# Performance work log

Measured on AMD Instinct MI355X. Metric: run time of the kernel, lower is better.

Reference implementation:

```python
import jax, jax.numpy as jnp
import numpy as np

N = 131072      # total nodes across batched graphs
E = 524288      # total directed edges (avg degree 4, molecular graphs)
F_NODE = 64     # raw atom features
F_BOND = 16     # raw bond features
D = 128         # hidden width (hard-coded in the module)
H2 = 16
G = 4096        # number of graphs in the batch
DIM_OUT = 1


def _make_params(key):
    ks = iter(jax.random.split(key, 64))
    def w(shape, scale):
        return jax.random.normal(next(ks), shape, jnp.float32) * scale
    p = {"fc1_w": w((F_NODE, D), 0.1), "fc1_b": jnp.zeros((D,), jnp.float32)}
    for l in (1, 2, 3):
        p[f"gc{l}_wq"] = w((D, D), 0.05); p[f"gc{l}_bq"] = jnp.zeros((D,), jnp.float32)
        p[f"gc{l}_wk"] = w((D, D), 0.05); p[f"gc{l}_bk"] = jnp.zeros((D,), jnp.float32)
        p[f"gc{l}_wv"] = w((D, D), 0.05); p[f"gc{l}_bv"] = jnp.zeros((D,), jnp.float32)
        p[f"gc{l}_we"] = w((F_BOND, D), 0.05)   # PyG lin_edge has no bias
        p[f"gc{l}_ws"] = w((D, D), 0.05); p[f"gc{l}_bs"] = jnp.zeros((D,), jnp.float32)
    p["fc2_w"] = w((D, H2), 0.1); p["fc2_b"] = jnp.zeros((H2,), jnp.float32)
    p["fc3_w"] = w((H2, DIM_OUT), 0.1); p["fc3_b"] = jnp.zeros((DIM_OUT,), jnp.float32)
    return p


def setup_inputs() -> dict:
    key = jax.random.key(0)
    k1, k2, k3, k4, kp = jax.random.split(key, 5)
    inp = {
        "x": jax.random.normal(k1, (N, F_NODE), jnp.float32),
        "edge_index": jax.random.randint(k2, (2, E), 0, N),
        "edge_attr": jax.random.normal(k3, (E, F_BOND), jnp.float32),
        "batch": jnp.sort(jax.random.randint(k4, (N,), 0, G)),
    }
    inp.update(_make_params(kp))
    return inp


def _tconv(x, src, dst, edge_attr, wq, bq, wk, bk, wv, bv, we, ws, bs):
    # PyG TransformerConv, heads=1, concat=True, beta=False, root_weight=True
    n = x.shape[0]
    q = x @ wq + bq                                   # [N,D]
    k = x @ wk + bk                                   # [N,D]
    v = x @ wv + bv                                   # [N,D]
    e = edge_attr @ we                                # [E,D] edge projection
    kj = k[src] + e                                   # key_j + edge
    vj = v[src] + e                                   # value_j + edge
    alpha = jnp.sum(q[dst] * kj, axis=-1) / jnp.sqrt(jnp.float32(D))   # [E]
    # segment softmax over incoming edges of each dst node
    amax = jax.ops.segment_max(alpha, dst, num_segments=n)
    ex = jnp.exp(alpha - amax[dst])
    denom = jax.ops.segment_sum(ex, dst, num_segments=n)
    w = ex / denom[dst]                               # [E]
    agg = jax.ops.segment_sum(vj * w[:, None], dst, num_segments=n)    # scatter-add
    return agg + x @ ws + bs                          # skip / root weight


def reference(x, edge_index, edge_attr, batch,
              fc1_w, fc1_b,
              gc1_wq, gc1_bq, gc1_wk, gc1_bk, gc1_wv, gc1_bv, gc1_we, gc1_ws, gc1_bs,
              gc2_wq, gc2_bq, gc2_wk, gc2_bk, gc2_wv, gc2_bv, gc2_we, gc2_ws, gc2_bs,
              gc3_wq, gc3_bq, gc3_wk, gc3_bk, gc3_wv, gc3_bv, gc3_we, gc3_ws, gc3_bs,
              fc2_w, fc2_b, fc3_w, fc3_b):
    src, dst = edge_index[0], edge_index[1]
    h = x @ fc1_w + fc1_b
    layers = [
        (gc1_wq, gc1_bq, gc1_wk, gc1_bk, gc1_wv, gc1_bv, gc1_we, gc1_ws, gc1_bs),
        (gc2_wq, gc2_bq, gc2_wk, gc2_bk, gc2_wv, gc2_bv, gc2_we, gc2_ws, gc2_bs),
        (gc3_wq, gc3_bq, gc3_wk, gc3_bk, gc3_wv, gc3_bv, gc3_we, gc3_ws, gc3_bs),
    ]
    for p in layers:
        h = jax.nn.relu(_tconv(h, src, dst, edge_attr, *p))
    # global mean pool over graph ids
    cnt = jax.ops.segment_sum(jnp.ones((h.shape[0],), h.dtype), batch, num_segments=G)
    hg = jax.ops.segment_sum(h, batch, num_segments=G) / jnp.maximum(cnt, 1.0)[:, None]
    h = jax.nn.relu(hg @ fc2_w + fc2_b)
    return h @ fc3_w + fc3_b                          # [G, DIM_OUT]
```

## Files before the change

### kernel.cpp

```cpp
#include <hip/hip_runtime.h>
#include <hip/hip_fp16.h>


#define D 128

typedef _Float16 half8 __attribute__((ext_vector_type(8)));
typedef float f32x4 __attribute__((ext_vector_type(4)));

__global__ __launch_bounds__(256) void hist_kernel(const int* __restrict__ dst,
                                                   int* __restrict__ counts, int e) {
  int i = blockIdx.x * 256 + threadIdx.x;
  if (i < e) atomicAdd(&counts[dst[i]], 1);
}

__global__ __launch_bounds__(256) void scan_a_kernel(const int* __restrict__ counts,
                                                     int* __restrict__ incl,
                                                     int* __restrict__ bsum) {
  int gid = blockIdx.x * 256 + threadIdx.x;
  int lane = threadIdx.x & 63, wid = threadIdx.x >> 6;
  int v = counts[gid];
  int s = v;
  #pragma unroll
  for (int off = 1; off < 64; off <<= 1) {
    int t = __shfl_up(s, off, 64);
    if (lane >= off) s += t;
  }
  __shared__ int wsum[4];
  if (lane == 63) wsum[wid] = s;
  __syncthreads();
  #pragma unroll
  for (int w = 0; w < 3; ++w)
    if (wid > w) s += wsum[w];
  incl[gid] = s;
  if (threadIdx.x == 255) bsum[blockIdx.x] = s;
}

__global__ __launch_bounds__(512) void scan_b_kernel(int* __restrict__ bs) {
  int tid = threadIdx.x;
  int lane = tid & 63, wid = tid >> 6;
  int v = bs[tid];
  int s = v;
  #pragma unroll
  for (int off = 1; off < 64; off <<= 1) {
    int t = __shfl_up(s, off, 64);
    if (lane >= off) s += t;
  }
  __shared__ int wsum[8];
  if (lane == 63) wsum[wid] = s;
  __syncthreads();
  #pragma unroll
  for (int w = 0; w < 7; ++w)
    if (wid > w) s += wsum[w];
  bs[tid] = s - v;
}

__global__ __launch_bounds__(256) void scan_c_kernel(const int* __restrict__ incl,
                                                     const int* __restrict__ counts,
                                                     const int* __restrict__ bsum,
                                                     int* __restrict__ offs, int n, int e) {
  int gid = blockIdx.x * 256 + threadIdx.x;
  if (gid < n) offs[gid] = incl[gid] - counts[gid] + bsum[blockIdx.x];
  if (gid == 0) offs[n] = e;
}

__global__ __launch_bounds__(256) void scatter_kernel(const int* __restrict__ srcs,
                                                      const int* __restrict__ dsts,
                                                      const int* __restrict__ offs,
                                                      int* __restrict__ cursor,
                                                      int* __restrict__ csr_src,
                                                      int* __restrict__ csr_eid, int e) {
  int i = blockIdx.x * 256 + threadIdx.x;
  if (i >= e) return;
  int d = dsts[i];
  int slot = atomicAdd(&cursor[d], 1);
  int p = offs[d] + slot;
  csr_src[p] = srcs[i];
  csr_eid[p] = i;
}

__global__ __launch_bounds__(256) void sort_kernel(const int* __restrict__ offs,
                                                   int* __restrict__ eid,
                                                   int* __restrict__ srcs, int n) {
  int i = blockIdx.x * 256 + threadIdx.x;
  if (i >= n) return;
  int b = offs[i], e = offs[i + 1];
  for (int p = b + 1; p < e; ++p) {
    int ke = eid[p], ks = srcs[p];
    int q = p - 1;
    while (q >= b && eid[q] > ke) {
      eid[q + 1] = eid[q]; srcs[q + 1] = srcs[q]; --q;
    }
    eid[q + 1] = ke; srcs[q + 1] = ks;
  }
}

__global__ __launch_bounds__(256) void convw_kernel(const float* __restrict__ W,
                                                    __half* __restrict__ out,
                                                    int ncols, int K) {
  int idx = blockIdx.x * 256 + threadIdx.x;
  if (idx >= ncols * K) return;
  int n = idx / K, kk = idx - n * K;
  out[idx] = __float2half(W[(size_t)kk * ncols + n]);
}

__global__ __launch_bounds__(256) void convwe_kernel(const float* __restrict__ we,
                                                     const float* __restrict__ Wq,
                                                     const float* __restrict__ bq,
                                                     __half* __restrict__ outW,
                                                     float* __restrict__ outB) {
  int idx = blockIdx.x * 256 + threadIdx.x;
  if (idx < 2048) {
    int f = idx >> 7, kk = idx & 127;
    float s = 0.f;
    for (int d = 0; d < 128; ++d) s += we[f * 128 + d] * Wq[kk * 128 + d];
    outW[f * 128 + kk] = __float2half(s);
  } else if (idx < 2064) {
    int f = idx - 2048;
    float s = 0.f;
    for (int d = 0; d < 128; ++d) s += we[f * 128 + d] * bq[d];
    outB[f] = s;
  }
}

__global__ __launch_bounds__(256) void bcat_kernel(const float* __restrict__ bq,
                                                   const float* __restrict__ bk,
                                                   const float* __restrict__ bv,
                                                   const float* __restrict__ bs,
                                                   float* __restrict__ out) {
  int j = blockIdx.x * 256 + threadIdx.x;
  if (j >= 512) return;
  const float* src = (j < 128) ? bq : (j < 256) ? bk : (j < 384) ? bv : bs;
  out[j] = src[j & 127];
}

__device__ inline void store4h(__half* p, float4 v) {
  __half2 h01 = __floats2half2_rn(v.x, v.y);
  __half2 h23 = __floats2half2_rn(v.z, v.w);
  uint2 u;
  u.x = *(unsigned int*)&h01;
  u.y = *(unsigned int*)&h23;
  *(uint2*)p = u;
}

__device__ inline void load8h(const __half* p, float4& lo, float4& hi) {
  uint4 u = *(const uint4*)p;
  float2 a = __half22float2(*(__half2*)&u.x);
  float2 b = __half22float2(*(__half2*)&u.y);
  float2 c = __half22float2(*(__half2*)&u.z);
  float2 d = __half22float2(*(__half2*)&u.w);
  lo = make_float4(a.x, a.y, b.x, b.y);
  hi = make_float4(c.x, c.y, d.x, d.y);
}

template <int K, int NCT, bool QKVS>
__global__ __launch_bounds__(256) void mfma_gemm_kernel(
    const float* in, const __half* __restrict__ Wt, const float* __restrict__ bias,
    __half* __restrict__ oq, __half* __restrict__ ok, __half* __restrict__ ov,
    float* os, float* __restrict__ qt) {
  constexpr int WST = K + 8;
  __shared__ alignas(16) __half Wc[128 * WST];
  const int tid = threadIdx.x;
  const int w = tid >> 6, l = tid & 63;
  const int lo = l & 15, hi = l >> 4;
  const size_t row = (size_t)blockIdx.x * 64 + w * 16 + lo;

  half8 af[K / 32];
  #pragma unroll
  for (int s = 0; s < K / 32; ++s) {
    const float* sp = in + row * K + s * 32 + hi * 8;
    float4 f0 = *(const float4*)sp;
    float4 f1 = *(const float4*)(sp + 4);
    half8 a;
    a[0] = (_Float16)f0.x; a[1] = (_Float16)f0.y; a[2] = (_Float16)f0.z; a[3] = (_Float16)f0.w;
    a[4] = (_Float16)f1.x; a[5] = (_Float16)f1.y; a[6] = (_Float16)f1.z; a[7] = (_Float16)f1.w;
    af[s] = a;
  }

  #pragma unroll 1
  for (int ch = 0; ch < NCT / 8; ++ch) {
    __syncthreads();
    #pragma unroll
    for (int i = 0; i < 128 * K / 8 / 256; ++i) {
      int idx = i * 256 + tid;
      int col = idx / (K / 8), kk = (idx % (K / 8)) * 8;
      *(uint4*)&Wc[col * WST + kk] =
          *(const uint4*)(Wt + (size_t)(ch * 128 + col) * K + kk);
    }
    __syncthreads();

    #pragma unroll
    for (int t = 0; t < 8; ++t) {
      f32x4 c = {0.f, 0.f, 0.f, 0.f};
      #pragma unroll
      for (int s = 0; s < K / 32; ++s) {
        half8 bf = *(const half8*)&Wc[(t * 16 + lo) * WST + s * 32 + hi * 8];
        c = __builtin_amdgcn_mfma_f32_16x16x32_f16(bf, af[s], c, 0, 0, 0);
      }
      const int col0 = ch * 128 + t * 16 + hi * 4;
      float4 b4 = *(const float4*)(bias + col0);
      float4 o;
      o.x = c[0] + b4.x; o.y = c[1] + b4.y; o.z = c[2] + b4.z; o.w = c[3] + b4.w;
      if (QKVS) {
        const int mid = col0 >> 7, cc = col0 & 127;
        if (mid == 0)      store4h(oq + row * 128 + cc, o);
        else if (mid == 1) store4h(ok + row * 128 + cc, o);
        else if (mid == 2) store4h(ov + row * 128 + cc, o);
        else               *(float4*)(os + row * 128 + cc) = o;
      } else {
        *(float4*)(os + row * 128 + col0) = o;
      }
    }
  }

  if constexpr (QKVS) {
    __syncthreads();
    {
      int col = tid >> 4;
      int kk = (tid & 15) * 8;
      *(uint4*)&Wc[col * WST + kk] =
          *(const uint4*)(Wt + (size_t)(512 + col) * K + kk);
    }
    __syncthreads();
    f32x4 c = {0.f, 0.f, 0.f, 0.f};
    #pragma unroll
    for (int s = 0; s < K / 32; ++s) {
      half8 bf = *(const half8*)&Wc[lo * WST + s * 32 + hi * 8];
      c = __builtin_amdgcn_mfma_f32_16x16x32_f16(bf, af[s], c, 0, 0, 0);
    }
    float4 b4 = *(const float4*)(bias + 512 + hi * 4);
    float4 o;
    o.x = c[0] + b4.x; o.y = c[1] + b4.y; o.z = c[2] + b4.z; o.w = c[3] + b4.w;
    *(float4*)(qt + row * 16 + hi * 4) = o;
  }
}

__global__ __launch_bounds__(256) void node_kernel(
    const __half* __restrict__ q, const __half* __restrict__ k, const __half* __restrict__ v,
    float* __restrict__ h, const float* __restrict__ edge_attr,
    const float* __restrict__ we, const float* __restrict__ tq,
    const int* __restrict__ offs, const int* __restrict__ csr_src,
    const int* __restrict__ csr_eid) {
  __shared__ float we_s[16 * 128];
  for (int i = threadIdx.x; i < (16 * 128) / 4; i += 256)
    ((float4*)we_s)[i] = ((const float4*)we)[i];
  __syncthreads();

  const int lane = threadIdx.x & 63;
  const int wid = threadIdx.x >> 6;
  const int g = lane >> 4, sub = lane & 15;
  const int node = blockIdx.x * 16 + wid * 4 + g;
  const int d0 = sub * 8;
  const float inv_sqrt_d = 0.08838834764831845f;

  float4 qlo, qhi;
  load8h(q + (size_t)node * D + d0, qlo, qhi);
  float4 slo = *(const float4*)(h + (size_t)node * D + d0);
  float4 shi = *(const float4*)(h + (size_t)node * D + d0 + 4);
  const float tf = tq[(size_t)node * 16 + sub];

  const int eb = offs[node], ee = offs[node + 1];
  float m = -3.0e38f, den = 0.f, accE = 0.f;
  float4 alo = {0.f, 0.f, 0.f, 0.f}, ahi = {0.f, 0.f, 0.f, 0.f};

  float4 klon = {0,0,0,0}, khin = {0,0,0,0}, vlon = {0,0,0,0}, vhin = {0,0,0,0};
  float eafn = 0.f;
  int p = eb;
  if (p < ee) {
    int src = csr_src[p];
    int eid = csr_eid[p];
    load8h(k + (size_t)src * D + d0, klon, khin);
    load8h(v + (size_t)src * D + d0, vlon, vhin);
    eafn = edge_attr[(size_t)eid * 16 + sub];
  }
  while (p < ee) {
    float4 klo = klon, khi = khin, vlo = vlon, vhi = vhin;
    float eaf = eafn;
    ++p;
    if (p < ee) {
      int src = csr_src[p];
      int eid = csr_eid[p];
      load8h(k + (size_t)src * D + d0, klon, khin);
      load8h(v + (size_t)src * D + d0, vlon, vhin);
      eafn = edge_attr[(size_t)eid * 16 + sub];
    }
    float pa = qlo.x * klo.x + qlo.y * klo.y + qlo.z * klo.z + qlo.w * klo.w +
               qhi.x * khi.x + qhi.y * khi.y + qhi.z * khi.z + qhi.w * khi.w +
               eaf * tf;
    #pragma unroll
    for (int off = 8; off > 0; off >>= 1) pa += __shfl_xor(pa, off, 64);
    pa *= inv_sqrt_d;
    float mn = fmaxf(m, pa);
    float esc = __expf(m - mn);
    float ew = __expf(pa - mn);
    den = den * esc + ew;
    alo.x = alo.x * esc + ew * vlo.x;
    alo.y = alo.y * esc + ew * vlo.y;
    alo.z = alo.z * esc + ew * vlo.z;
    alo.w = alo.w * esc + ew * vlo.w;
    ahi.x = ahi.x * esc + ew * vhi.x;
    ahi.y = ahi.y * esc + ew * vhi.y;
    ahi.z = ahi.z * esc + ew * vhi.z;
    ahi.w = ahi.w * esc + ew * vhi.w;
    accE = accE * esc + ew * eaf;
    m = mn;
  }

  if (den > 0.f) {
    float inv = 1.0f / den;
    float4 elo = {0.f, 0.f, 0.f, 0.f}, ehi = {0.f, 0.f, 0.f, 0.f};
    const int gbase = lane & 48;
    #pragma unroll
    for (int f = 0; f < 16; ++f) {
      float aE = __shfl(accE, gbase + f, 64);
      float4 w0 = *(const float4*)&we_s[f * 128 + d0];
      float4 w1 = *(const float4*)&we_s[f * 128 + d0 + 4];
      elo.x += aE * w0.x; elo.y += aE * w0.y; elo.z += aE * w0.z; elo.w += aE * w0.w;
      ehi.x += aE * w1.x; ehi.y += aE * w1.y; ehi.z += aE * w1.z; ehi.w += aE * w1.w;
    }
    slo.x += (alo.x + elo.x) * inv;
    slo.y += (alo.y + elo.y) * inv;
    slo.z += (alo.z + elo.z) * inv;
    slo.w += (alo.w + elo.w) * inv;
    shi.x += (ahi.x + ehi.x) * inv;
    shi.y += (ahi.y + ehi.y) * inv;
    shi.z += (ahi.z + ehi.z) * inv;
    shi.w += (ahi.w + ehi.w) * inv;
  }
  slo.x = fmaxf(slo.x, 0.f); slo.y = fmaxf(slo.y, 0.f);
  slo.z = fmaxf(slo.z, 0.f); slo.w = fmaxf(slo.w, 0.f);
  shi.x = fmaxf(shi.x, 0.f); shi.y = fmaxf(shi.y, 0.f);
  shi.z = fmaxf(shi.z, 0.f); shi.w = fmaxf(shi.w, 0.f);
  *(float4*)(h + (size_t)node * D + d0) = slo;
  *(float4*)(h + (size_t)node * D + d0 + 4) = shi;
}

__global__ __launch_bounds__(64) void pool_kernel(const float* __restrict__ h,
                                                  const int* __restrict__ batch,
                                                  float* __restrict__ hg,
                                                  float* __restrict__ cnt, int n) {
  int base = blockIdx.x * 128;
  int lane = threadIdx.x;
  float2 acc = {0.f, 0.f};
  float run = 0.f;
  int cur = batch[base];
  for (int i = 0; i < 128; ++i) {
    int node = base + i;
    int g = batch[node];
    if (g != cur) {
      atomicAdd(&hg[(size_t)cur * D + 2 * lane], acc.x);
      atomicAdd(&hg[(size_t)cur * D + 2 * lane + 1], acc.y);
      if (lane == 0) atomicAdd(&cnt[cur], run);
      acc.x = acc.y = 0.f; run = 0.f; cur = g;
    }
    float2 hv = *(const float2*)(h + (size_t)node * D + 2 * lane);
    acc.x += hv.x; acc.y += hv.y; run += 1.f;
  }
  atomicAdd(&hg[(size_t)cur * D + 2 * lane], acc.x);
  atomicAdd(&hg[(size_t)cur * D + 2 * lane + 1], acc.y);
  if (lane == 0) atomicAdd(&cnt[cur], run);
}

__global__ __launch_bounds__(256) void head_kernel(const float* __restrict__ hg,
                                                   const float* __restrict__ cnt,
                                                   const float* __restrict__ w2,
                                                   const float* __restrict__ b2,
                                                   const float* __restrict__ w3,
                                                   const float* __restrict__ b3,
                                                   float* __restrict__ out) {
  __shared__ float w2s[128 * 16];
  __shared__ float rowb[4][128];
  for (int i = threadIdx.x; i < (128 * 16) / 4; i += 256)
    ((float4*)w2s)[i] = ((const float4*)w2)[i];
  int wid = threadIdx.x >> 6, lane = threadIdx.x & 63;
  int g = blockIdx.x * 4 + wid;
  float inv = 1.0f / fmaxf(cnt[g], 1.0f);
  rowb[wid][lane] = hg[(size_t)g * D + lane] * inv;
  rowb[wid][lane + 64] = hg[(size_t)g * D + 64 + lane] * inv;
  __syncthreads();
  float t = 0.f;
  if (lane < 16) {
    float a = b2[lane];
    for (int d = 0; d < 128; ++d) a += rowb[wid][d] * w2s[d * 16 + lane];
    t = fmaxf(a, 0.f) * w3[lane];
  }
  #pragma unroll
  for (int off = 8; off > 0; off >>= 1) t += __shfl_xor(t, off, 64);
  if (lane == 0) out[g] = t + b3[0];
}

extern "C" void kernel_launch(void* const* d_in, const int* in_sizes, int n_in,
                              void* d_out, int out_size, void* d_ws, size_t ws_size,
                              hipStream_t stream) {
  const float* x = (const float*)d_in[0];
  const int* eidx = (const int*)d_in[1];
  const float* eattr = (const float*)d_in[2];
  const int* batch = (const int*)d_in[3];
  const float* fc1_w = (const float*)d_in[4];
  const float* fc1_b = (const float*)d_in[5];
  const float* WQ[3] = {(const float*)d_in[6], (const float*)d_in[15], (const float*)d_in[24]};
  const float* BQ[3] = {(const float*)d_in[7], (const float*)d_in[16], (const float*)d_in[25]};
  const float* WK[3] = {(const float*)d_in[8], (const float*)d_in[17], (const float*)d_in[26]};
  const float* BK[3] = {(const float*)d_in[9], (const float*)d_in[18], (const float*)d_in[27]};
  const float* WV[3] = {(const float*)d_in[10], (const float*)d_in[19], (const float*)d_in[28]};
  const float* BV[3] = {(const float*)d_in[11], (const float*)d_in[20], (const float*)d_in[29]};
  const float* WE[3] = {(const float*)d_in[12], (const float*)d_in[21], (const float*)d_in[30]};
  const float* WS[3] = {(const float*)d_in[13], (const float*)d_in[22], (const float*)d_in[31]};
  const float* BS[3] = {(const float*)d_in[14], (const float*)d_in[23], (const float*)d_in[32]};
  const float* fc2_w = (const float*)d_in[33];
  const float* fc2_b = (const float*)d_in[34];
  const float* fc3_w = (const float*)d_in[35];
  const float* fc3_b = (const float*)d_in[36];

  const int N = in_sizes[0] / 64;
  const int E = in_sizes[1] / 2;
  const int G = out_size;
  const int* srcs = eidx;
  const int* dsts = eidx + E;
  const size_t ND = (size_t)N * D;

  char* base = (char*)d_ws;
  size_t off = 0;
  auto alloc = [&](size_t bytes) {
    void* p = base + off;
    off = (off + bytes + 255) & ~(size_t)255;
    return p;
  };
  float* hg = (float*)alloc((size_t)G * D * 4);
  float* cntf = (float*)alloc((size_t)G * 4);
  int* counts = (int*)alloc((size_t)N * 4);
  int* cursor = (int*)alloc((size_t)N * 4);
  size_t zero_bytes = (size_t)G * D * 4 + (size_t)G * 4 + 2 * (size_t)N * 4;
  int* incl = (int*)alloc((size_t)N * 4);
  int* offs = (int*)alloc((size_t)(N + 4) * 4);
  int* bsum = (int*)alloc(512 * 4);
  int* csr_src = (int*)alloc((size_t)E * 4);
  int* csr_eid = (int*)alloc((size_t)E * 4);
  float* h = (float*)alloc(ND * 4);
  __half* q = (__half*)alloc(ND * 2);
  __half* k = (__half*)alloc(ND * 2);
  __half* v = (__half*)alloc(ND * 2);
  float* qt = (float*)alloc((size_t)N * 16 * 4);
  __half* Wt[3];
  float* bc[3];
  for (int l = 0; l < 3; ++l) {
    Wt[l] = (__half*)alloc(528 * 128 * 2);
    bc[l] = (float*)alloc(544 * 4);
  }
  __half* fc1t = (__half*)alloc(128 * 64 * 2);
  if (off > ws_size) return;

  hipMemsetAsync(hg, 0, zero_bytes, stream);

  for (int l = 0; l < 3; ++l) {
    convw_kernel<<<64, 256, 0, stream>>>(WQ[l], Wt[l] + 0 * 16384, 128, 128);
    convw_kernel<<<64, 256, 0, stream>>>(WK[l], Wt[l] + 1 * 16384, 128, 128);
    convw_kernel<<<64, 256, 0, stream>>>(WV[l], Wt[l] + 2 * 16384, 128, 128);
    convw_kernel<<<64, 256, 0, stream>>>(WS[l], Wt[l] + 3 * 16384, 128, 128);
    convwe_kernel<<<9, 256, 0, stream>>>(WE[l], WQ[l], BQ[l],
                                         Wt[l] + 4 * 16384, bc[l] + 512);
    bcat_kernel<<<2, 256, 0, stream>>>(BQ[l], BK[l], BV[l], BS[l], bc[l]);
  }
  convw_kernel<<<32, 256, 0, stream>>>(fc1_w, fc1t, 128, 64);

  hist_kernel<<<E / 256, 256, 0, stream>>>(dsts, counts, E);
  scan_a_kernel<<<N / 256, 256, 0, stream>>>(counts, incl, bsum);
  scan_b_kernel<<<1, 512, 0, stream>>>(bsum);
  scan_c_kernel<<<N / 256, 256, 0, stream>>>(incl, counts, bsum, offs, N, E);
  scatter_kernel<<<E / 256, 256, 0, stream>>>(srcs, dsts, offs, cursor, csr_src, csr_eid, E);
  sort_kernel<<<N / 256, 256, 0, stream>>>(offs, csr_eid, csr_src, N);

  mfma_gemm_kernel<64, 8, false><<<N / 64, 256, 0, stream>>>(
      x, fc1t, fc1_b, nullptr, nullptr, nullptr, h, nullptr);

  for (int l = 0; l < 3; ++l) {
    mfma_gemm_kernel<128, 32, true><<<N / 64, 256, 0, stream>>>(
        h, Wt[l], bc[l], q, k, v, h, qt);
    node_kernel<<<N / 16, 256, 0, stream>>>(q, k, v, h, eattr, WE[l], qt,
                                            offs, csr_src, csr_eid);
  }

  pool_kernel<<<N / 128, 64, 0, stream>>>(h, batch, hg, cntf, N);
  head_kernel<<<G / 4, 256, 0, stream>>>(hg, cntf, fc2_w, fc2_b, fc3_w, fc3_b, (float*)d_out);
}
```

Before: 609.3 us.

## Interleave QKV storage, degree-sort nodes, and pad edge-weight smem layout

Stores Q, K and V interleaved per node in one buffer so each gathered source row keeps K and V next to each other. Adds a counting sort of nodes by in-degree (capped at 31) to build a permutation, and node_kernel processes nodes in that order so the four nodes sharing a wave have similar edge counts and less divergence. It also pads the edge-weight table in shared memory to a stride of 10 floats per 8-column group, aiming to cut bank conflicts. The cost is extra preprocessing kernels and scattered node reads and writes through the permutation.

Measured after the change: 1.694 ms. 178% more time.

```diff
diff --git a/kernel.cpp b/kernel.cpp
--- a/kernel.cpp
+++ b/kernel.cpp
@@ -92,6 +92,35 @@
     }
     eid[q + 1] = ke; srcs[q + 1] = ks;
   }
+}
+
+__global__ __launch_bounds__(256) void hist_deg_kernel(const int* __restrict__ counts,
+                                                       int* __restrict__ hist32, int n) {
+  int i = blockIdx.x * 256 + threadIdx.x;
+  if (i < n) atomicAdd(&hist32[min(counts[i], 31)], 1);
+}
+
+__global__ __launch_bounds__(64) void scan32_kernel(int* __restrict__ h) {
+  int lane = threadIdx.x;
+  int v = (lane < 32) ? h[lane] : 0;
+  int s = v;
+  #pragma unroll
+  for (int off = 1; off < 32; off <<= 1) {
+    int t = __shfl_up(s, off, 64);
+    if (lane >= off) s += t;
+  }
+  if (lane < 32) h[lane] = s - v;
+}
+
+__global__ __launch_bounds__(256) void scatter_deg_kernel(const int* __restrict__ counts,
+                                                          const int* __restrict__ hist32,
+                                                          int* __restrict__ hcur32,
+                                                          int* __restrict__ perm, int n) {
+  int i = blockIdx.x * 256 + threadIdx.x;
+  if (i >= n) return;
+  int b = min(counts[i], 31);
+  int pos = hist32[b] + atomicAdd(&hcur32[b], 1);
+  perm[pos] = i;
 }
 
 __global__ __launch_bounds__(256) void convw_kernel(const float* __restrict__ W,
@@ -155,8 +184,7 @@
 template <int K, int NCT, bool QKVS>
 __global__ __launch_bounds__(256) void mfma_gemm_kernel(
     const float* in, const __half* __restrict__ Wt, const float* __restrict__ bias,
-    __half* __restrict__ oq, __half* __restrict__ ok, __half* __restrict__ ov,
-    float* os, float* __restrict__ qt) {
+    __half* __restrict__ qkv, float* os, float* __restrict__ qt) {
   constexpr int WST = K + 8;
   __shared__ alignas(16) __half Wc[128 * WST];
   const int tid = threadIdx.x;
@@ -202,10 +230,8 @@
       o.x = c[0] + b4.x; o.y = c[1] + b4.y; o.z = c[2] + b4.z; o.w = c[3] + b4.w;
       if (QKVS) {
         const int mid = col0 >> 7, cc = col0 & 127;
-        if (mid == 0)      store4h(oq + row * 128 + cc, o);
-        else if (mid == 1) store4h(ok + row * 128 + cc, o);
-        else if (mid == 2) store4h(ov + row * 128 + cc, o);
-        else               *(float4*)(os + row * 128 + cc) = o;
+        if (mid < 3) store4h(qkv + row * 384 + mid * 128 + cc, o);
+        else         *(float4*)(os + row * 128 + cc) = o;
       } else {
         *(float4*)(os + row * 128 + col0) = o;
       }
@@ -235,30 +261,32 @@
 }
 
 __global__ __launch_bounds__(256) void node_kernel(
-    const __half* __restrict__ q, const __half* __restrict__ k, const __half* __restrict__ v,
-    float* __restrict__ h, const float* __restrict__ edge_attr,
+    const __half* __restrict__ qkv, float* __restrict__ h,
+    const float* __restrict__ edge_attr,
     const float* __restrict__ we, const float* __restrict__ tq,
     const int* __restrict__ offs, const int* __restrict__ csr_src,
-    const int* __restrict__ csr_eid) {
-  __shared__ float we_s[16 * 128];
-  for (int i = threadIdx.x; i < (16 * 128) / 4; i += 256)
-    ((float4*)we_s)[i] = ((const float4*)we)[i];
+    const int* __restrict__ csr_eid, const int* __restrict__ perm) {
+  __shared__ float we_s[16 * 160];
+  for (int i = threadIdx.x; i < 2048; i += 256) {
+    int f = i >> 7, d = i & 127;
+    we_s[f * 160 + (d >> 3) * 10 + (d & 7)] = we[i];
+  }
   __syncthreads();
 
   const int lane = threadIdx.x & 63;
   const int wid = threadIdx.x >> 6;
   const int g = lane >> 4, sub = lane & 15;
-  const int node = blockIdx.x * 16 + wid * 4 + g;
+  const int nid = perm[blockIdx.x * 16 + wid * 4 + g];
   const int d0 = sub * 8;
   const float inv_sqrt_d = 0.08838834764831845f;
 
   float4 qlo, qhi;
-  load8h(q + (size_t)node * D + d0, qlo, qhi);
-  float4 slo = *(const float4*)(h + (size_t)node * D + d0);
-  float4 shi = *(const float4*)(h + (size_t)node * D + d0 + 4);
-  const float tf = tq[(size_t)node * 16 + sub];
-
-  const int eb = offs[node], ee = offs[node + 1];
+  load8h(qkv + (size_t)nid * 384 + d0, qlo, qhi);
+  float4 slo = *(const float4*)(h + (size_t)nid * D + d0);
+  float4 shi = *(const float4*)(h + (size_t)nid * D + d0 + 4);
+  const float tf = tq[(size_t)nid * 16 + sub];
+
+  const int eb = offs[nid], ee = offs[nid + 1];
   float m = -3.0e38f, den = 0.f, accE = 0.f;
   float4 alo = {0.f, 0.f, 0.f, 0.f}, ahi = {0.f, 0.f, 0.f, 0.f};
 
@@ -268,8 +296,8 @@
   if (p < ee) {
     int src = csr_src[p];
     int eid = csr_eid[p];
-    load8h(k + (size_t)src * D + d0, klon, khin);
-    load8h(v + (size_t)src * D + d0, vlon, vhin);
+    load8h(qkv + (size_t)src * 384 + 128 + d0, klon, khin);
+    load8h(qkv + (size_t)src * 384 + 256 + d0, vlon, vhin);
     eafn = edge_attr[(size_t)eid * 16 + sub];
   }
   while (p < ee) {
@@ -279,8 +307,8 @@
     if (p < ee) {
       int src = csr_src[p];
       int eid = csr_eid[p];
-      load8h(k + (size_t)src * D + d0, klon, khin);
-      load8h(v + (size_t)src * D + d0, vlon, vhin);
+      load8h(qkv + (size_t)src * 384 + 128 + d0, klon, khin);
+      load8h(qkv + (size_t)src * 384 + 256 + d0, vlon, vhin);
       eafn = edge_attr[(size_t)eid * 16 + sub];
     }
     float pa = qlo.x * klo.x + qlo.y * klo.y + qlo.z * klo.z + qlo.w * klo.w +
@@ -309,13 +337,17 @@
     float inv = 1.0f / den;
     float4 elo = {0.f, 0.f, 0.f, 0.f}, ehi = {0.f, 0.f, 0.f, 0.f};
     const int gbase = lane & 48;
+    const int wb = sub * 10;
     #pragma unroll
     for (int f = 0; f < 16; ++f) {
       float aE = __shfl(accE, gbase + f, 64);
-      float4 w0 = *(const float4*)&we_s[f * 128 + d0];
-      float4 w1 = *(const float4*)&we_s[f * 128 + d0 + 4];
-      elo.x += aE * w0.x; elo.y += aE * w0.y; elo.z += aE * w0.z; elo.w += aE * w0.w;
-      ehi.x += aE * w1.x; ehi.y += aE * w1.y; ehi.z += aE * w1.z; ehi.w += aE * w1.w;
+      const float* wr = &we_s[f * 160 + wb];
+      float2 w01 = *(const float2*)(wr + 0);
+      float2 w23 = *(const float2*)(wr + 2);
+      float2 w45 = *(const float2*)(wr + 4);
+      float2 w67 = *(const float2*)(wr + 6);
+      elo.x += aE * w01.x; elo.y += aE * w01.y; elo.z += aE * w23.x; elo.w += aE * w23.y;
+      ehi.x += aE * w45.x; ehi.y += aE * w45.y; ehi.z += aE * w67.x; ehi.w += aE * w67.y;
     }
     slo.x += (alo.x + elo.x) * inv;
     slo.y += (alo.y + elo.y) * inv;
@@ -330,8 +362,8 @@
   slo.z = fmaxf(slo.z, 0.f); slo.w = fmaxf(slo.w, 0.f);
   shi.x = fmaxf(shi.x, 0.f); shi.y = fmaxf(shi.y, 0.f);
   shi.z = fmaxf(shi.z, 0.f); shi.w = fmaxf(shi.w, 0.f);
-  *(float4*)(h + (size_t)node * D + d0) = slo;
-  *(float4*)(h + (size_t)node * D + d0 + 4) = shi;
+  *(float4*)(h + (size_t)nid * D + d0) = slo;
+  *(float4*)(h + (size_t)nid * D + d0 + 4) = shi;
 }
 
 __global__ __launch_bounds__(64) void pool_kernel(const float* __restrict__ h,
@@ -429,16 +461,17 @@
   float* cntf = (float*)alloc((size_t)G * 4);
   int* counts = (int*)alloc((size_t)N * 4);
   int* cursor = (int*)alloc((size_t)N * 4);
-  size_t zero_bytes = (size_t)G * D * 4 + (size_t)G * 4 + 2 * (size_t)N * 4;
+  int* hist32 = (int*)alloc(32 * 4);
+  int* hcur32 = (int*)alloc(32 * 4);
+  size_t zero_bytes = off;
   int* incl = (int*)alloc((size_t)N * 4);
   int* offs = (int*)alloc((size_t)(N + 4) * 4);
   int* bsum = (int*)alloc(512 * 4);
   int* csr_src = (int*)alloc((size_t)E * 4);
   int* csr_eid = (int*)alloc((size_t)E * 4);
+  int* perm = (int*)alloc((size_t)N * 4);
   float* h = (float*)alloc(ND * 4);
-  __half* q = (__half*)alloc(ND * 2);
-  __half* k = (__half*)alloc(ND * 2);
-  __half* v = (__half*)alloc(ND * 2);
+  __half* qkv = (__half*)alloc((size_t)N * 384 * 2);
   float* qt = (float*)alloc((size_t)N * 16 * 4);
   __half* Wt[3];
   float* bc[3];
@@ -463,6 +496,9 @@
   convw_kernel<<<32, 256, 0, stream>>>(fc1_w, fc1t, 128, 64);
 
   hist_kernel<<<E / 256, 256, 0, stream>>>(dsts, counts, E);
+  hist_deg_kernel<<<N / 256, 256, 0, stream>>>(counts, hist32, N);
+  scan32_kernel<<<1, 64, 0, stream>>>(hist32);
+  scatter_deg_kernel<<<N / 256, 256, 0, stream>>>(counts, hist32, hcur32, perm, N);
   scan_a_kernel<<<N / 256, 256, 0, stream>>>(counts, incl, bsum);
   scan_b_kernel<<<1, 512, 0, stream>>>(bsum);
   scan_c_kernel<<<N / 256, 256, 0, stream>>>(incl, counts, bsum, offs, N, E);
@@ -470,13 +506,13 @@
   sort_kernel<<<N / 256, 256, 0, stream>>>(offs, csr_eid, csr_src, N);
 
   mfma_gemm_kernel<64, 8, false><<<N / 64, 256, 0, stream>>>(
-      x, fc1t, fc1_b, nullptr, nullptr, nullptr, h, nullptr);
+      x, fc1t, fc1_b, nullptr, h, nullptr);
 
   for (int l = 0; l < 3; ++l) {
     mfma_gemm_kernel<128, 32, true><<<N / 64, 256, 0, stream>>>(
-        h, Wt[l], bc[l], q, k, v, h, qt);
-    node_kernel<<<N / 16, 256, 0, stream>>>(q, k, v, h, eattr, WE[l], qt,
-                                            offs, csr_src, csr_eid);
+        h, Wt[l], bc[l], qkv, h, qt);
+    node_kernel<<<N / 16, 256, 0, stream>>>(qkv, h, eattr, WE[l], qt,
+                                            offs, csr_src, csr_eid, perm);
   }
 
   pool_kernel<<<N / 128, 64, 0, stream>>>(h, batch, hg, cntf, N);
```
